# Kernel optimization log

Hardware: AMD Instinct MI355X
Metric: run time of the kernel (lower is better)

## Reference

```python
import jax, jax.numpy as jnp
import numpy as np

B, S, D, H, P = 4, 4096, 1024, 8, 32
K = D // H  # head_dim = 128


def setup_inputs() -> dict:
    key = jax.random.key(0)
    ks = jax.random.split(key, 12)
    f = lambda k, shape, s: jax.random.normal(k, shape, dtype=jnp.float32) * s
    return {
        "x": f(ks[0], (B, S, D), 1.0),
        "W_proj": f(ks[1], (H, K, D), 0.03),
        "resonance_freqs": f(ks[2], (H, K), 0.01),
        "pol_W": f(ks[3], (H, P, K), 0.08),
        "pol_b": jnp.zeros((H, P), jnp.float32),
        "imp_W1": f(ks[4], (16, 1), 0.5),               # Linear(1, 16)
        "imp_b1": jnp.zeros((16,), jnp.float32),
        "imp_W2": f(ks[5], (1, 16), 0.25),              # Linear(16, 1)
        "imp_b2": jnp.zeros((1,), jnp.float32),
        "out_W": f(ks[6], (D, D), 0.03),                # Linear(dim, dim)
        "out_b": jnp.zeros((D,), jnp.float32),
        "ln_g": jnp.ones((D,), jnp.float32),
        "ln_b": jnp.zeros((D,), jnp.float32),
        "causal": 1,
    }


def reference(x, W_proj, resonance_freqs, pol_W, pol_b, imp_W1, imp_b1,
              imp_W2, imp_b2, out_W, out_b, ln_g, ln_b, causal):
    Bx, Sx, Dx = x.shape
    nH = W_proj.shape[0]
    # per-head projection + resonance frequency modulation -> (B, H, S, K)
    heads = jnp.einsum('bsd,hkd->bhsk', x, W_proj)
    heads = heads * jnp.cos(resonance_freqs * jnp.pi)[None, :, None, :]

    # --- GuaXiangDuiChong: learned cross-head impedance ---
    summary = heads.mean(axis=2)                                   # (B, H, K)
    pol = jnp.tanh(jnp.einsum('bhk,hpk->bhp', summary, pol_W) + pol_b[None])
    pol = pol / jnp.maximum(jnp.linalg.norm(pol, axis=-1, keepdims=True), 1e-12)
    dots = jnp.einsum('bhp,bgp->bhg', pol, pol)                    # (B, H, H)
    z = dots[..., None]                                            # (B, H, H, 1)
    hid = jax.nn.gelu(z * imp_W1[:, 0] + imp_b1, approximate=False)  # (B, H, H, 16)
    imp = jax.nn.softplus(jnp.einsum('bijc,oc->bijo', hid, imp_W2) + imp_b2)[..., 0]
    eye = jnp.eye(nH, dtype=x.dtype)
    impedance = imp * (1.0 - eye)                                  # (B, H, H)

    # --- cross-head transfer ---
    # h_i += sum_{j != i} heads_j / (1 + imp[i,j]) * 0.1, causally mean-masked.
    coef = (0.1 / (1.0 + impedance)) * (1.0 - eye)                 # zero diagonal (i == j skipped)
    transfer = jnp.einsum('bij,bjsk->bisk', coef, heads)           # (B, H, S, K)
    if causal and Sx > 1:
        # masked_fill(t>s)+mean over t of a key-independent tensor == scale by (s+1)/S
        scale = (jnp.arange(Sx, dtype=x.dtype) + 1.0) / Sx
        transfer = transfer * scale[None, None, :, None]
    out_heads = heads + transfer

    merged = out_heads.transpose(0, 2, 1, 3).reshape(Bx, Sx, Dx)   # cat heads on last dim
    y = merged @ out_W.T + out_b + x                               # dropout is identity in eval
    mu = y.mean(-1, keepdims=True)
    var = ((y - mu) ** 2).mean(-1, keepdims=True)
    normed = (y - mu) / jnp.sqrt(var + 1e-5) * ln_g + ln_b
    return normed, impedance
```

## Files before the change

kernel.cpp:

```cpp
#include <hip/hip_runtime.h>

typedef __bf16 bf16x8 __attribute__((ext_vector_type(8)));
typedef float f32x4 __attribute__((ext_vector_type(4)));
typedef unsigned short us8 __attribute__((ext_vector_type(8)));

#define PI_F 3.14159265358979323846f

__device__ __forceinline__ unsigned short f2bf(float f) {
    unsigned u = __float_as_uint(f);
    u += 0x7FFFu + ((u >> 16) & 1u);
    return (unsigned short)(u >> 16);
}
__device__ __forceinline__ float bf2f(unsigned short h) {
    return __uint_as_float(((unsigned)h) << 16);
}

__device__ __forceinline__ void async16(const void* g, void* l) {
    __builtin_amdgcn_global_load_lds(
        (const __attribute__((address_space(1))) unsigned int*)g,
        (__attribute__((address_space(3))) unsigned int*)l, 16, 0, 0);
}

__global__ __launch_bounds__(256) void prep_k(const float* __restrict__ W,
                                              const float* __restrict__ fr,
                                              const float* __restrict__ Wo,
                                              unsigned short* __restrict__ W1b,
                                              unsigned short* __restrict__ Wob) {
    int idx = blockIdx.x * 256 + threadIdx.x;
    if (idx < (1 << 20)) {
        int n = idx >> 10, d = idx & 1023;
        int k = n >> 3, h = n & 7;
        float c = cosf(fr[h * 128 + k] * PI_F);
        W1b[idx] = f2bf(W[((h * 128 + k) << 10) + d] * c);
    } else {
        int i2 = idx - (1 << 20);
        int n = i2 >> 10, dp = i2 & 1023;
        int k = dp >> 3, h = dp & 7;
        Wob[i2] = f2bf(Wo[(n << 10) + h * 128 + k]);
    }
}

__global__ __launch_bounds__(256) void xbar_cast(const float* __restrict__ x,
                                                 unsigned short* __restrict__ xb,
                                                 float* __restrict__ part) {
    int bid = blockIdx.x;
    int b = bid >> 8;
    int s0 = (bid & 255) * 16;
    int t = threadIdx.x;
    float a0 = 0.f, a1 = 0.f, a2 = 0.f, a3 = 0.f;
    for (int i = 0; i < 16; ++i) {
        long row = (long)b * 4096 + s0 + i;
        float4 v = ((const float4*)x)[row * 256 + t];
        a0 += v.x; a1 += v.y; a2 += v.z; a3 += v.w;
        ushort4 u;
        u.x = f2bf(v.x); u.y = f2bf(v.y); u.z = f2bf(v.z); u.w = f2bf(v.w);
        ((ushort4*)xb)[row * 256 + t] = u;
    }
    float4 p; p.x = a0; p.y = a1; p.z = a2; p.w = a3;
    ((float4*)part)[bid * 256 + t] = p;
}

__global__ __launch_bounds__(256) void xbar_r(const float* __restrict__ part,
                                              float* __restrict__ xbar) {
    __shared__ float sl[256];
    int blk = blockIdx.x;
    int b = blk >> 3, dgrp = blk & 7;
    int t = threadIdx.x;
    int col = dgrp * 128 + (t & 127);
    int ih = t >> 7;
    float s = 0.f;
    for (int i = 0; i < 128; ++i) {
        int cb = b * 256 + ih * 128 + i;
        s += part[cb * 1024 + col];
    }
    sl[t] = s;
    __syncthreads();
    if (t < 128) xbar[b * 1024 + col] = sl[t] + sl[t + 128];
}

__global__ __launch_bounds__(256) void summary_k(const float* __restrict__ xbar,
                                                 const float* __restrict__ W,
                                                 const float* __restrict__ fr,
                                                 float* __restrict__ summary) {
    int wave = (blockIdx.x * 256 + threadIdx.x) >> 6;
    int lane = threadIdx.x & 63;
    int b = wave >> 10, hk = wave & 1023;
    int h = hk >> 7, k = hk & 127;
    const float* wrow = &W[(h * 128 + k) << 10];
    const float* xrow = &xbar[b << 10];
    float s = 0.f;
    for (int d = lane; d < 1024; d += 64) s += xrow[d] * wrow[d];
    for (int off = 32; off; off >>= 1) s += __shfl_down(s, off);
    if (lane == 0) {
        float c = cosf(fr[h * 128 + k] * PI_F);
        summary[wave] = s * c * (1.0f / 4096.0f);
    }
}

__global__ __launch_bounds__(256) void imp_k(const float* __restrict__ summary,
                                             const float* __restrict__ pol_W,
                                             const float* __restrict__ pol_b,
                                             const float* __restrict__ imp_W1,
                                             const float* __restrict__ imp_b1,
                                             const float* __restrict__ imp_W2,
                                             const float* __restrict__ imp_b2,
                                             float* __restrict__ coef_out,
                                             float* __restrict__ imp_out) {
    __shared__ float pol[4][8][32];
    __shared__ float rn[32];
    int t = threadIdx.x;
    for (int o = t; o < 1024; o += 256) {
        int b = o >> 8, h = (o >> 5) & 7, p = o & 31;
        const float* srow = &summary[(b * 8 + h) * 128];
        const float* wrow = &pol_W[(h * 32 + p) * 128];
        float acc = pol_b[h * 32 + p];
        for (int k = 0; k < 128; ++k) acc += srow[k] * wrow[k];
        pol[b][h][p] = tanhf(acc);
    }
    __syncthreads();
    if (t < 32) {
        int b = t >> 3, h = t & 7;
        float ss = 0.f;
        for (int p = 0; p < 32; ++p) { float v = pol[b][h][p]; ss += v * v; }
        rn[t] = 1.0f / fmaxf(sqrtf(ss), 1e-12f);
    }
    __syncthreads();
    {
        int b = t >> 6, i = (t >> 3) & 7, j = t & 7;
        float d = 0.f;
        for (int p = 0; p < 32; ++p) d += pol[b][i][p] * pol[b][j][p];
        d *= rn[b * 8 + i] * rn[b * 8 + j];
        float s = imp_b2[0];
        for (int c = 0; c < 16; ++c) {
            float z = d * imp_W1[c] + imp_b1[c];
            float gl = 0.5f * z * (1.0f + erff(z * 0.70710678118654752f));
            s += gl * imp_W2[c];
        }
        float sp = fmaxf(s, 0.0f) + log1pf(expf(-fabsf(s)));
        float impv = (i == j) ? 0.0f : sp;
        imp_out[t] = impv;
        coef_out[t] = (i == j) ? 0.0f : 0.1f / (1.0f + impv);
    }
}

__device__ __forceinline__ void swizzle_blk(int n, long& rowBase, long& colBase) {
    int xcd = n & 7, s = n >> 3;
    rowBase = (long)(xcd * 16 + (s & 15)) * 128;
    colBase = (long)(s >> 4) * 128;
}

#define GEMM_CORE(A_, B_, As_, Bs_)                                            \
    const int wave = t >> 6;                                                   \
    const int lane = t & 63;                                                   \
    const int wr = wave >> 1, wc = wave & 1;                                   \
    const int lr = lane >> 2;                                                  \
    const int lb = (lane & 3) * 16;                                            \
    const char* gA = (const char*)A_ + (rowBase + wave * 32 + lr) * 2048 + lb; \
    const char* gB = (const char*)B_ + (colBase + wave * 32 + lr) * 2048 + lb; \
    char* lA = (char*)As_ + wave * 2048;                                       \
    char* lB = (char*)Bs_ + wave * 2048;                                       \
    const int q = lane >> 4;                                                   \
    const int c16 = lane & 15;                                                 \
    f32x4 acc[4][4] = {};                                                      \
    for (int kt = 0; kt < 1024; kt += 32) {                                    \
        const char* a0 = gA + kt * 2;                                          \
        const char* b0 = gB + kt * 2;                                          \
        async16(a0, lA);                                                       \
        async16(a0 + 16 * 2048, lA + 1024);                                    \
        async16(b0, lB);                                                       \
        async16(b0 + 16 * 2048, lB + 1024);                                    \
        __syncthreads();                                                       \
        bf16x8 af[4], bfr[4];                                                  \
        _Pragma("unroll")                                                      \
        for (int mi = 0; mi < 4; ++mi)                                         \
            af[mi] = *(const bf16x8*)((const char*)As_ +                       \
                       ((wr * 64 + mi * 16 + c16) * 32 + q * 8) * 2);          \
        _Pragma("unroll")                                                      \
        for (int ni = 0; ni < 4; ++ni)                                         \
            bfr[ni] = *(const bf16x8*)((const char*)Bs_ +                      \
                       ((wc * 64 + ni * 16 + c16) * 32 + q * 8) * 2);          \
        _Pragma("unroll")                                                      \
        for (int mi = 0; mi < 4; ++mi)                                         \
            _Pragma("unroll")                                                  \
            for (int ni = 0; ni < 4; ++ni)                                     \
                acc[mi][ni] = __builtin_amdgcn_mfma_f32_16x16x32_bf16(         \
                    af[mi], bfr[ni], acc[mi][ni], 0, 0, 0);                    \
        __syncthreads();                                                       \
    }

__global__ __launch_bounds__(256, 3) void gemm1_mix(const unsigned short* __restrict__ A,
                                                    const unsigned short* __restrict__ B,
                                                    const float* __restrict__ coef,
                                                    const int* __restrict__ causal,
                                                    unsigned short* __restrict__ C) {
    __shared__ char smem[16384];
    __shared__ float cfs[64];
    unsigned short* As = (unsigned short*)smem;
    unsigned short* Bs = (unsigned short*)(smem + 8192);
    float* mixt = (float*)smem;
    const int t = threadIdx.x;
    long rowBase, colBase;
    swizzle_blk(blockIdx.x, rowBase, colBase);
    const int b = (int)(rowBase >> 12);
    if (t < 64) cfs[t] = coef[b * 64 + t];
    const int causalv = causal[0];

    GEMM_CORE(A, B, As, Bs)

    const int r16 = t >> 4, kg = t & 15;
#pragma unroll
    for (int p = 0; p < 8; ++p) {
        if (wr == (p >> 2)) {
            int mi = p & 3;
#pragma unroll
            for (int ni = 0; ni < 4; ++ni)
#pragma unroll
                for (int r = 0; r < 4; ++r)
                    mixt[(q * 4 + r) * 132 + wc * 64 + ni * 16 + c16] = acc[mi][ni][r];
        }
        __syncthreads();
        const float* src = mixt + r16 * 132 + kg * 8;
        float v[8];
#pragma unroll
        for (int j = 0; j < 8; ++j) v[j] = src[j];
        long row = rowBase + p * 16 + r16;
        float scale = causalv ? (float)((row & 4095) + 1) * (1.0f / 4096.0f) : 1.0f;
        us8 o;
#pragma unroll
        for (int i = 0; i < 8; ++i) {
            float ts = 0.f;
#pragma unroll
            for (int j = 0; j < 8; ++j) ts += cfs[i * 8 + j] * v[j];
            o[i] = f2bf(v[i] + scale * ts);
        }
        *(us8*)(C + row * 1024 + colBase + kg * 8) = o;
        __syncthreads();
    }
}

__global__ __launch_bounds__(256, 3) void gemm_bt(const unsigned short* __restrict__ A,
                                                  const unsigned short* __restrict__ B,
                                                  unsigned short* __restrict__ C) {
    __shared__ unsigned short As[128 * 32];
    __shared__ unsigned short Bs[128 * 32];
    const int t = threadIdx.x;
    long rowBase, colBase;
    swizzle_blk(blockIdx.x, rowBase, colBase);

    GEMM_CORE(A, B, As, Bs)

#pragma unroll
    for (int mi = 0; mi < 4; ++mi) {
#pragma unroll
        for (int ni = 0; ni < 4; ++ni) {
            long col = colBase + wc * 64 + ni * 16 + c16;
            long row0 = rowBase + wr * 64 + mi * 16 + q * 4;
#pragma unroll
            for (int r = 0; r < 4; ++r)
                C[(row0 + r) * 1024 + col] = f2bf(acc[mi][ni][r]);
        }
    }
}

__global__ __launch_bounds__(256) void ln_k(const unsigned short* __restrict__ ypre,
                                            const float* __restrict__ x,
                                            const float* __restrict__ outb,
                                            const float* __restrict__ gam,
                                            const float* __restrict__ bet,
                                            float* __restrict__ out) {
    int row = blockIdx.x;
    int t = threadIdx.x;
    long base = (long)row * 1024 + t * 4;
    ushort4 yp = *(const ushort4*)(ypre + base);
    float4 xv = *(const float4*)(x + base);
    float4 bv = *(const float4*)(outb + t * 4);
    float y0 = bf2f(yp.x) + xv.x + bv.x;
    float y1 = bf2f(yp.y) + xv.y + bv.y;
    float y2 = bf2f(yp.z) + xv.z + bv.z;
    float y3 = bf2f(yp.w) + xv.w + bv.w;
    float s = y0 + y1 + y2 + y3;
    float ss = y0 * y0 + y1 * y1 + y2 * y2 + y3 * y3;
    for (int off = 32; off; off >>= 1) {
        s += __shfl_down(s, off);
        ss += __shfl_down(ss, off);
    }
    __shared__ float red[8];
    int wv = t >> 6, ln = t & 63;
    if (ln == 0) { red[wv] = s; red[4 + wv] = ss; }
    __syncthreads();
    float S1 = red[0] + red[1] + red[2] + red[3];
    float S2 = red[4] + red[5] + red[6] + red[7];
    float mu = S1 * (1.0f / 1024.0f);
    float var = S2 * (1.0f / 1024.0f) - mu * mu;
    float rs = 1.0f / sqrtf(var + 1e-5f);
    float4 gv = *(const float4*)(gam + t * 4);
    float4 bb = *(const float4*)(bet + t * 4);
    float4 o;
    o.x = (y0 - mu) * rs * gv.x + bb.x;
    o.y = (y1 - mu) * rs * gv.y + bb.y;
    o.z = (y2 - mu) * rs * gv.z + bb.z;
    o.w = (y3 - mu) * rs * gv.w + bb.w;
    *(float4*)(out + base) = o;
}

extern "C" void kernel_launch(void* const* d_in, const int* in_sizes, int n_in,
                              void* d_out, int out_size, void* d_ws, size_t ws_size,
                              hipStream_t stream) {
    const float* x       = (const float*)d_in[0];
    const float* W_proj  = (const float*)d_in[1];
    const float* freqs   = (const float*)d_in[2];
    const float* pol_W   = (const float*)d_in[3];
    const float* pol_b   = (const float*)d_in[4];
    const float* imp_W1  = (const float*)d_in[5];
    const float* imp_b1  = (const float*)d_in[6];
    const float* imp_W2  = (const float*)d_in[7];
    const float* imp_b2  = (const float*)d_in[8];
    const float* out_W   = (const float*)d_in[9];
    const float* out_b   = (const float*)d_in[10];
    const float* ln_g    = (const float*)d_in[11];
    const float* ln_b    = (const float*)d_in[12];
    const int*   causal  = (const int*)d_in[13];
    float* out = (float*)d_out;

    char* ws = (char*)d_ws;
    unsigned short* xb      = (unsigned short*)(ws + 0);
    unsigned short* merged  = (unsigned short*)(ws + 33554432);
    unsigned short* w1b     = (unsigned short*)(ws + 67108864);
    unsigned short* wob     = (unsigned short*)(ws + 69206016);
    float* xbar             = (float*)(ws + 71303168);
    float* summary          = (float*)(ws + 71319552);
    float* coef             = (float*)(ws + 71335936);
    float* part             = (float*)merged;
    unsigned short* ypre    = xb;

    prep_k<<<8192, 256, 0, stream>>>(W_proj, freqs, out_W, w1b, wob);
    xbar_cast<<<1024, 256, 0, stream>>>(x, xb, part);
    xbar_r<<<32, 256, 0, stream>>>(part, xbar);
    summary_k<<<1024, 256, 0, stream>>>(xbar, W_proj, freqs, summary);
    imp_k<<<1, 256, 0, stream>>>(summary, pol_W, pol_b, imp_W1, imp_b1,
                                 imp_W2, imp_b2, coef, out + 16777216);
    gemm1_mix<<<1024, 256, 0, stream>>>(xb, w1b, coef, causal, merged);
    gemm_bt<<<1024, 256, 0, stream>>>(merged, wob, ypre);
    ln_k<<<16384, 256, 0, stream>>>(ypre, x, out_b, ln_g, ln_b, out);
}
```

Before: 299.6 us.

## Rewrite GEMMs as 256x256 tiles with multi-stage async LDS pipeline

Both GEMM kernels move from 128x128 tiles on 256 threads to 256x256 tiles on 512 threads (8 waves). The K loop now runs over a 4-slot LDS ring fed by direct global-to-LDS async loads, with explicit vmcnt waits and raw barriers instead of a load-then-sync-per-step loop. MFMA bursts run at raised wave priority, so loads for later K steps overlap with compute. This aims to hide memory latency and improve operand reuse. In exchange it uses 128KB of LDS per block, launches only 256 blocks, and raises register pressure, which lowers occupancy.

```diff
diff --git a/kernel.cpp b/kernel.cpp
--- a/kernel.cpp
+++ b/kernel.cpp
@@ -143,123 +143,170 @@
     }
 }
 
-__device__ __forceinline__ void swizzle_blk(int n, long& rowBase, long& colBase) {
+#define VMCNT(n) asm volatile("s_waitcnt vmcnt(" #n ")" ::: "memory")
+#define NOPW ((void)0)
+#define SBAR() __builtin_amdgcn_s_barrier()
+
+__device__ __forceinline__ void swz256(int n, long& rowBase, long& colBase) {
     int xcd = n & 7, s = n >> 3;
-    rowBase = (long)(xcd * 16 + (s & 15)) * 128;
-    colBase = (long)(s >> 4) * 128;
-}
-
-#define GEMM_CORE(A_, B_, As_, Bs_)                                            \
-    const int wave = t >> 6;                                                   \
-    const int lane = t & 63;                                                   \
-    const int wr = wave >> 1, wc = wave & 1;                                   \
-    const int lr = lane >> 2;                                                  \
-    const int lb = (lane & 3) * 16;                                            \
-    const char* gA = (const char*)A_ + (rowBase + wave * 32 + lr) * 2048 + lb; \
-    const char* gB = (const char*)B_ + (colBase + wave * 32 + lr) * 2048 + lb; \
-    char* lA = (char*)As_ + wave * 2048;                                       \
-    char* lB = (char*)Bs_ + wave * 2048;                                       \
-    const int q = lane >> 4;                                                   \
-    const int c16 = lane & 15;                                                 \
-    f32x4 acc[4][4] = {};                                                      \
-    for (int kt = 0; kt < 1024; kt += 32) {                                    \
-        const char* a0 = gA + kt * 2;                                          \
-        const char* b0 = gB + kt * 2;                                          \
-        async16(a0, lA);                                                       \
-        async16(a0 + 16 * 2048, lA + 1024);                                    \
-        async16(b0, lB);                                                       \
-        async16(b0 + 16 * 2048, lB + 1024);                                    \
-        __syncthreads();                                                       \
-        bf16x8 af[4], bfr[4];                                                  \
-        _Pragma("unroll")                                                      \
-        for (int mi = 0; mi < 4; ++mi)                                         \
-            af[mi] = *(const bf16x8*)((const char*)As_ +                       \
-                       ((wr * 64 + mi * 16 + c16) * 32 + q * 8) * 2);          \
-        _Pragma("unroll")                                                      \
-        for (int ni = 0; ni < 4; ++ni)                                         \
-            bfr[ni] = *(const bf16x8*)((const char*)Bs_ +                      \
-                       ((wc * 64 + ni * 16 + c16) * 32 + q * 8) * 2);          \
-        _Pragma("unroll")                                                      \
-        for (int mi = 0; mi < 4; ++mi)                                         \
-            _Pragma("unroll")                                                  \
-            for (int ni = 0; ni < 4; ++ni)                                     \
-                acc[mi][ni] = __builtin_amdgcn_mfma_f32_16x16x32_bf16(         \
-                    af[mi], bfr[ni], acc[mi][ni], 0, 0, 0);                    \
-        __syncthreads();                                                       \
-    }
-
-__global__ __launch_bounds__(256, 3) void gemm1_mix(const unsigned short* __restrict__ A,
-                                                    const unsigned short* __restrict__ B,
-                                                    const float* __restrict__ coef,
-                                                    const int* __restrict__ causal,
-                                                    unsigned short* __restrict__ C) {
-    __shared__ char smem[16384];
+    rowBase = (long)(xcd * 8 + (s & 7)) * 256;
+    colBase = (long)(s >> 3) * 256;
+}
+
+#define STG(sPtr, dPtr, koff, slot)                                          \
+    async16((sPtr) + (koff), (dPtr) + (slot) * 16384);                       \
+    async16((sPtr) + (koff) + 262144, (dPtr) + (slot) * 16384 + 8192);
+
+#define DS_A(h, slot)                                                        \
+    _Pragma("unroll") for (int i_ = 0; i_ < 4; ++i_)                         \
+        af[i_] = *(const bf16x8*)(rdA + (slot) * 16384 + ((h) * 4 + i_) * 1024);
+
+#define DS_B(slot)                                                           \
+    _Pragma("unroll") for (int i_ = 0; i_ < 4; ++i_)                         \
+        bf[i_] = *(const bf16x8*)(rdB + (slot) * 16384 + i_ * 1024);
+
+#define MF(h)                                                                \
+    __builtin_amdgcn_s_setprio(1);                                           \
+    _Pragma("unroll") for (int i_ = 0; i_ < 4; ++i_)                         \
+        _Pragma("unroll") for (int j_ = 0; j_ < 4; ++j_)                     \
+            acc[(h) * 4 + i_][j_] = __builtin_amdgcn_mfma_f32_16x16x32_bf16( \
+                af[i_], bf[j_], acc[(h) * 4 + i_][j_], 0, 0, 0);             \
+    __builtin_amdgcn_s_setprio(0);
+
+#define GROUP(R0, R1, S0, S1, DO_ST, KNXT, VM_MID, VM_END)                   \
+    {                                                                        \
+        bf16x8 af[4], bf[4];                                                 \
+        DS_A(0, R0) DS_B(R0)                                                 \
+        if (DO_ST) { STG(sA, stDstA, (KNXT), S0) }                           \
+        SBAR(); MF(0) SBAR();                                                \
+        DS_A(1, R0)                                                          \
+        if (DO_ST) { STG(sB, stDstB, (KNXT), S0) }                           \
+        VM_MID; SBAR(); MF(1) SBAR();                                        \
+        DS_A(0, R1) DS_B(R1)                                                 \
+        if (DO_ST) { STG(sA, stDstA, (KNXT) + 64, S1) }                      \
+        SBAR(); MF(0) SBAR();                                                \
+        DS_A(1, R1)                                                          \
+        if (DO_ST) { STG(sB, stDstB, (KNXT) + 64, S1) }                      \
+        VM_END; SBAR(); MF(1) SBAR();                                        \
+    }
+
+__device__ __forceinline__ void gemm8_core(const char* gAB, const char* gBB,
+                                           char* smem, const int t,
+                                           f32x4 acc[8][4]) {
+    const int l = t & 63, wid = t >> 6;
+    const int wm = wid >> 2, wn = wid & 3;
+    const long stOff = (long)((wid << 4) + (t & 15)) * 2048 + ((t >> 4) & 3) * 16;
+    const char* sA = gAB + stOff;
+    const char* sB = gBB + stOff;
+    char* As = smem;
+    char* Bs = smem + 65536;
+    char* stDstA = As + wid * 1024;
+    char* stDstB = Bs + wid * 1024;
+    const char* rdA = As + wm * 8192 + l * 16;
+    const char* rdB = Bs + wn * 4096 + l * 16;
+
+    STG(sA, stDstA, 0, 0)
+    STG(sB, stDstB, 0, 0)
+    STG(sA, stDstA, 64, 1)
+    STG(sB, stDstB, 64, 1)
+    VMCNT(4);
+    SBAR();
+
+    int kb = 128;
+    for (int it = 0; it < 7; ++it) {
+        GROUP(0, 1, 2, 3, true, kb, VMCNT(4), VMCNT(4))
+        GROUP(2, 3, 0, 1, true, kb + 128, VMCNT(4), VMCNT(4))
+        kb += 256;
+    }
+    GROUP(0, 1, 2, 3, true, 1920, VMCNT(4), VMCNT(4))
+    GROUP(2, 3, 0, 1, false, 0, VMCNT(0), NOPW)
+}
+
+__global__ __launch_bounds__(512, 2) void gemm1_mix(
+    const unsigned short* __restrict__ A, const unsigned short* __restrict__ B,
+    const float* __restrict__ coef, const int* __restrict__ causal,
+    unsigned short* __restrict__ C) {
+    __shared__ char smem[131072];
     __shared__ float cfs[64];
-    unsigned short* As = (unsigned short*)smem;
-    unsigned short* Bs = (unsigned short*)(smem + 8192);
-    float* mixt = (float*)smem;
     const int t = threadIdx.x;
     long rowBase, colBase;
-    swizzle_blk(blockIdx.x, rowBase, colBase);
+    swz256(blockIdx.x, rowBase, colBase);
     const int b = (int)(rowBase >> 12);
     if (t < 64) cfs[t] = coef[b * 64 + t];
     const int causalv = causal[0];
 
-    GEMM_CORE(A, B, As, Bs)
-
-    const int r16 = t >> 4, kg = t & 15;
+    f32x4 acc[8][4] = {};
+    gemm8_core((const char*)A + rowBase * 2048, (const char*)B + colBase * 2048,
+               smem, t, acc);
+
+    const int l = t & 63, wid = t >> 6;
+    const int wm = wid >> 2, wn = wid & 3;
+    const int q = l >> 4, c16 = l & 15;
+    float* slab = (float*)smem;
 #pragma unroll
     for (int p = 0; p < 8; ++p) {
-        if (wr == (p >> 2)) {
-            int mi = p & 3;
-#pragma unroll
-            for (int ni = 0; ni < 4; ++ni)
-#pragma unroll
-                for (int r = 0; r < 4; ++r)
-                    mixt[(q * 4 + r) * 132 + wc * 64 + ni * 16 + c16] = acc[mi][ni][r];
+        if (wm == (p >> 2)) {
+            const int m0 = (p & 3) * 2;
+#pragma unroll
+            for (int m2 = 0; m2 < 2; ++m2)
+#pragma unroll
+                for (int ni = 0; ni < 4; ++ni)
+#pragma unroll
+                    for (int r = 0; r < 4; ++r)
+                        slab[(m2 * 16 + q * 4 + r) * 264 + wn * 64 + ni * 16 + c16] =
+                            acc[m0 + m2][ni][r];
         }
         __syncthreads();
-        const float* src = mixt + r16 * 132 + kg * 8;
-        float v[8];
-#pragma unroll
-        for (int j = 0; j < 8; ++j) v[j] = src[j];
-        long row = rowBase + p * 16 + r16;
-        float scale = causalv ? (float)((row & 4095) + 1) * (1.0f / 4096.0f) : 1.0f;
-        us8 o;
-#pragma unroll
-        for (int i = 0; i < 8; ++i) {
-            float ts = 0.f;
-#pragma unroll
-            for (int j = 0; j < 8; ++j) ts += cfs[i * 8 + j] * v[j];
-            o[i] = f2bf(v[i] + scale * ts);
+#pragma unroll
+        for (int gg = 0; gg < 2; ++gg) {
+            const int g = t + gg * 512;
+            const int row32 = g >> 5, kg = g & 31;
+            const float* src = slab + row32 * 264 + kg * 8;
+            float v[8];
+#pragma unroll
+            for (int j = 0; j < 8; ++j) v[j] = src[j];
+            const long row = rowBase + p * 32 + row32;
+            const float scale =
+                causalv ? (float)((row & 4095) + 1) * (1.0f / 4096.0f) : 1.0f;
+            us8 o;
+#pragma unroll
+            for (int i = 0; i < 8; ++i) {
+                float ts = 0.f;
+#pragma unroll
+                for (int j = 0; j < 8; ++j) ts += cfs[i * 8 + j] * v[j];
+                o[i] = f2bf(v[i] + scale * ts);
+            }
+            *(us8*)(C + row * 1024 + colBase + kg * 8) = o;
         }
-        *(us8*)(C + row * 1024 + colBase + kg * 8) = o;
         __syncthreads();
     }
 }
 
-__global__ __launch_bounds__(256, 3) void gemm_bt(const unsigned short* __restrict__ A,
+__global__ __launch_bounds__(512, 2) void gemm_bt(const unsigned short* __restrict__ A,
                                                   const unsigned short* __restrict__ B,
                                                   unsigned short* __restrict__ C) {
-    __shared__ unsigned short As[128 * 32];
-    __shared__ unsigned short Bs[128 * 32];
+    __shared__ char smem[131072];
     const int t = threadIdx.x;
     long rowBase, colBase;
-    swizzle_blk(blockIdx.x, rowBase, colBase);
-
-    GEMM_CORE(A, B, As, Bs)
-
-#pragma unroll
-    for (int mi = 0; mi < 4; ++mi) {
+    swz256(blockIdx.x, rowBase, colBase);
+
+    f32x4 acc[8][4] = {};
+    gemm8_core((const char*)A + rowBase * 2048, (const char*)B + colBase * 2048,
+               smem, t, acc);
+
+    const int l = t & 63, wid = t >> 6;
+    const int wm = wid >> 2, wn = wid & 3;
+    const int q = l >> 4, c16 = l & 15;
+#pragma unroll
+    for (int mi = 0; mi < 8; ++mi)
 #pragma unroll
         for (int ni = 0; ni < 4; ++ni) {
-            long col = colBase + wc * 64 + ni * 16 + c16;
-            long row0 = rowBase + wr * 64 + mi * 16 + q * 4;
+            const long col = colBase + wn * 64 + ni * 16 + c16;
+            const long row0 = rowBase + wm * 128 + mi * 16 + q * 4;
 #pragma unroll
             for (int r = 0; r < 4; ++r)
                 C[(row0 + r) * 1024 + col] = f2bf(acc[mi][ni][r]);
         }
-    }
 }
 
 __global__ __launch_bounds__(256) void ln_k(const unsigned short* __restrict__ ypre,
@@ -339,7 +386,7 @@
     summary_k<<<1024, 256, 0, stream>>>(xbar, W_proj, freqs, summary);
     imp_k<<<1, 256, 0, stream>>>(summary, pol_W, pol_b, imp_W1, imp_b1,
                                  imp_W2, imp_b2, coef, out + 16777216);
-    gemm1_mix<<<1024, 256, 0, stream>>>(xb, w1b, coef, causal, merged);
-    gemm_bt<<<1024, 256, 0, stream>>>(merged, wob, ypre);
+    gemm1_mix<<<256, 512, 0, stream>>>(xb, w1b, coef, causal, merged);
+    gemm_bt<<<256, 512, 0, stream>>>(merged, wob, ypre);
     ln_k<<<16384, 256, 0, stream>>>(ypre, x, out_b, ln_g, ln_b, out);
 }
```

New measurement: 298.4 us. Within noise of the previous version (-0.4%).
